# Kernel optimization log

Measured on AMD Instinct MI355X. Metric: run time of the kernel, lower is better.

Reference implementation:

```python
import jax, jax.numpy as jnp
import numpy as np

VARIANCE = (0.1, 0.2)
THRESHOLD = 0.5
NEG_POS = 3


def point_form(boxes):
    # (cx,cy,w,h) -> (xmin,ymin,xmax,ymax)
    return jnp.concatenate([boxes[:, :2] - boxes[:, 2:] / 2,
                            boxes[:, :2] + boxes[:, 2:] / 2], axis=1)


def jaccard(a, b):
    # a: [T,4] xyxy truths, b: [P,4] xyxy priors -> IoU [T,P]
    lt = jnp.maximum(a[:, None, :2], b[None, :, :2])
    rb = jnp.minimum(a[:, None, 2:], b[None, :, 2:])
    wh = jnp.clip(rb - lt, 0.0)
    inter = wh[..., 0] * wh[..., 1]
    area_a = ((a[:, 2] - a[:, 0]) * (a[:, 3] - a[:, 1]))[:, None]
    area_b = ((b[:, 2] - b[:, 0]) * (b[:, 3] - b[:, 1]))[None, :]
    return inter / (area_a + area_b - inter)


def encode(matched, priors):
    g_cxcy = (matched[:, :2] + matched[:, 2:]) / 2 - priors[:, :2]
    g_cxcy = g_cxcy / (VARIANCE[0] * priors[:, 2:])
    g_wh = jnp.log((matched[:, 2:] - matched[:, :2]) / priors[:, 2:]) / VARIANCE[1]
    return jnp.concatenate([g_cxcy, g_wh], axis=1)


def match_one(truths, priors):
    # SSD match for one image; labels are zeroed in BiBoxLoss -> binary conf {0,1}
    overlaps = jaccard(truths, point_form(priors))          # [T,P]
    best_prior_idx = jnp.argmax(overlaps, axis=1)           # [T]
    best_truth_overlap = jnp.max(overlaps, axis=0)          # [P]
    best_truth_idx = jnp.argmax(overlaps, axis=0)           # [P]
    best_truth_overlap = best_truth_overlap.at[best_prior_idx].set(2.0)
    best_truth_idx = best_truth_idx.at[best_prior_idx].set(
        jnp.arange(truths.shape[0]))
    matched = truths[best_truth_idx]                        # [P,4]
    conf = jnp.where(best_truth_overlap < THRESHOLD, 0, 1)  # [P] int
    loc = encode(matched, priors)
    return loc, conf


def bibox_loss(loc_data, conf_data, priors, targets):
    num, num_priors = loc_data.shape[0], loc_data.shape[1]
    truths = targets[..., :4]                               # [B,T,4]
    loc_t, conf_t = jax.vmap(lambda t: match_one(t, priors))(truths)

    pos = conf_t > 0                                        # [B,P]
    # smooth L1 (sum) over positive priors
    ad = jnp.abs(loc_data - loc_t)
    sl1 = jnp.where(ad < 1.0, 0.5 * ad * ad, ad - 0.5)
    loss_l = jnp.sum(sl1 * pos[..., None].astype(loc_data.dtype))

    # per-prior CE (logsumexp - gathered logit) for hard-negative mining
    lse = jax.nn.logsumexp(conf_data, axis=-1)              # [B,P]
    gathered = jnp.take_along_axis(conf_data, conf_t[..., None], axis=-1)[..., 0]
    loss_c_all = lse - gathered                             # [B,P]

    loss_c_mine = jnp.where(pos, 0.0, loss_c_all)
    loss_idx = jnp.argsort(-loss_c_mine, axis=1)
    idx_rank = jnp.argsort(loss_idx, axis=1)                # rank of each prior
    num_pos = jnp.sum(pos.astype(jnp.int32), axis=1, keepdims=True)  # [B,1]
    num_neg = jnp.minimum(NEG_POS * num_pos, num_priors - 1)
    neg = idx_rank < num_neg                                # [B,P]

    sel = pos | neg
    loss_c = jnp.sum(jnp.where(sel, loss_c_all, 0.0))

    N = jnp.sum(num_pos).astype(loc_data.dtype)
    return loss_l / N, loss_c / N


def setup_inputs() -> dict:
    key = jax.random.key(0)
    k1, k2, k3, k4, k5, k6 = jax.random.split(key, 6)
    B, P, T = 32, 65536, 16
    loc_data = jax.random.normal(k1, (B, P, 4), dtype=jnp.float32)
    conf_data = jax.random.normal(k2, (B, P, 2), dtype=jnp.float32)
    # priors: valid center-form boxes
    pc = 0.15 + 0.7 * jax.random.uniform(k3, (P, 2), dtype=jnp.float32)
    pwh = 0.05 + 0.25 * jax.random.uniform(k4, (P, 2), dtype=jnp.float32)
    priors = jnp.concatenate([pc, pwh], axis=1)
    # targets: valid corner-form boxes + dummy label column (zeroed by the loss)
    tc = 0.2 + 0.6 * jax.random.uniform(k5, (B, T, 2), dtype=jnp.float32)
    twh = 0.05 + 0.25 * jax.random.uniform(k6, (B, T, 2), dtype=jnp.float32)
    boxes = jnp.concatenate([tc - twh / 2, tc + twh / 2], axis=-1)
    targets = jnp.concatenate(
        [boxes, jnp.ones((B, T, 1), dtype=jnp.float32)], axis=-1)
    return {"loc_data": loc_data, "conf_data": conf_data,
            "priors": priors, "targets": targets}


def reference(loc_data, conf_data, priors, targets):
    return bibox_loss(loc_data, conf_data, priors, targets)
```

## Files before the change

### kernel.cpp

```cpp
#include <hip/hip_runtime.h>

#define NB_ 32
#define NP_ 65536
#define NT_ 16
#define HB 1024
#define HSCALE 128.0f
#define NBX 32
#define CHUNKS 2
#define BIAS 0xAAAAAAAAu

__device__ __forceinline__ float softplus_(float x) {
    return fmaxf(x, 0.0f) + __logf(1.0f + __expf(-fabsf(x)));
}

__device__ __forceinline__ float iou_fast(float tx0, float ty0, float tx1, float ty1, float ta,
                                          float bx0, float by0, float bx1, float by1, float ar) {
    float lx = fmaxf(tx0, bx0), ly = fmaxf(ty0, by0);
    float rx = fminf(tx1, bx1), ry = fminf(ty1, by1);
    float w = fmaxf(rx - lx, 0.0f), h = fmaxf(ry - ly, 0.0f);
    float inter = w * h;
    return __fdividef(inter, ta + ar - inter);
}

__global__ void __launch_bounds__(256) mainK(
    const float* __restrict__ loc, const float* __restrict__ conf,
    const float* __restrict__ priors, const float* __restrict__ targets,
    unsigned* __restrict__ hcnt, float* __restrict__ hsum,
    unsigned long long* __restrict__ bestPrior,
    float* __restrict__ sums_ll, float* __restrict__ sums_pc, unsigned* __restrict__ num_pos,
    float* __restrict__ final_l, float* __restrict__ final_c, unsigned* __restrict__ final_n,
    unsigned* __restrict__ bticket, unsigned* __restrict__ gticket,
    float* __restrict__ out)
{
    const int bx = blockIdx.x, b = blockIdx.y, tid = threadIdx.x;

    __shared__ float tr[NT_][5];
    __shared__ int hc[HB];
    __shared__ float hs[HB];
    __shared__ unsigned wkey[4][NT_], wp[4][NT_];
    __shared__ float sh_ll[4], sh_pc[4];
    __shared__ int sh_np[4];
    __shared__ unsigned ps[NT_];
    __shared__ float s_dll, s_dpc;
    __shared__ int s_dnp;
    __shared__ unsigned ccnt[16];
    __shared__ float csm[16];
    __shared__ int s_merge, s_lastg;

    for (int i = tid; i < HB; i += 256) { hc[i] = 0; hs[i] = 0.0f; }
    if (tid < NT_) {
        const float* tp = targets + ((size_t)b * NT_ + tid) * 5;
        float x0 = tp[0], y0 = tp[1], x1 = tp[2], y1 = tp[3];
        tr[tid][0] = x0; tr[tid][1] = y0; tr[tid][2] = x1; tr[tid][3] = y1;
        tr[tid][4] = (x1 - x0) * (y1 - y0);
    }
    __syncthreads();

    float ll_acc = 0.0f, pc_acc = 0.0f;
    int np_acc = 0;
    unsigned tkey[NT_];
#pragma unroll
    for (int t = 0; t < NT_; t++) tkey[t] = 0u;

    for (int c = 0; c < CHUNKS; c++) {
        const int pbase = (bx * CHUNKS + c) * 1024 + tid;
        float4 pr[4];
        float pbx0[4], pby0[4], pbx1[4], pby1[4], par[4];
#pragma unroll
        for (int i = 0; i < 4; i++) {
            pr[i] = ((const float4*)priors)[pbase + 256 * i];
            float hw = pr[i].z * 0.5f, hh = pr[i].w * 0.5f;
            pbx0[i] = pr[i].x - hw; pby0[i] = pr[i].y - hh;
            pbx1[i] = pr[i].x + hw; pby1[i] = pr[i].y + hh;
            par[i] = (pbx1[i] - pbx0[i]) * (pby1[i] - pby0[i]);
        }
        unsigned pkey[4] = {0u, 0u, 0u, 0u};
#pragma unroll
        for (int t = 0; t < NT_; t++) {
            float tx0 = tr[t][0], ty0 = tr[t][1], tx1 = tr[t][2], ty1 = tr[t][3], ta = tr[t][4];
            unsigned lowt = (unsigned)(15 - t);
            unsigned lowc = (unsigned)(15 - c * 4);
#pragma unroll
            for (int i = 0; i < 4; i++) {
                float iou = iou_fast(tx0, ty0, tx1, ty1, ta,
                                     pbx0[i], pby0[i], pbx1[i], pby1[i], par[i]);
                unsigned base = (__float_as_uint(iou) & 0xFFFFFFFCu) << 2;
                unsigned kt = base | lowt;
                unsigned kp = base | (lowc - (unsigned)i);
                pkey[i] = (kt > pkey[i]) ? kt : pkey[i];
                tkey[t] = (kp > tkey[t]) ? kp : tkey[t];
            }
        }
#pragma unroll
        for (int i = 0; i < 4; i++) {
            int p = pbase + 256 * i;
            size_t bp = (size_t)b * NP_ + p;
            bool pos = (pkey[i] >= 0xFC000000u);
            float2 cxy = ((const float2*)conf)[bp];
            float dd = cxy.y - cxy.x;
            float v = pos ? 0.0f : softplus_(dd);
            int bin = min(HB - 1, (int)(v * HSCALE));
            atomicAdd(&hc[bin], 1);
            atomicAdd(&hs[bin], v);
            if (pos) {
                np_acc++;
                pc_acc += softplus_(-dd);
                int t = 15 - (int)(pkey[i] & 15u);
                float tx0 = tr[t][0], ty0 = tr[t][1], tx1 = tr[t][2], ty1 = tr[t][3];
                float gcx = ((tx0 + tx1) * 0.5f - pr[i].x) / (0.1f * pr[i].z);
                float gcy = ((ty0 + ty1) * 0.5f - pr[i].y) / (0.1f * pr[i].w);
                float gw = __logf((tx1 - tx0) / pr[i].z) * 5.0f;
                float gh = __logf((ty1 - ty0) / pr[i].w) * 5.0f;
                float4 ld = ((const float4*)loc)[bp];
                float d0 = fabsf(ld.x - gcx), d1 = fabsf(ld.y - gcy);
                float d2 = fabsf(ld.z - gw),  d3 = fabsf(ld.w - gh);
                ll_acc += (d0 < 1.0f) ? 0.5f * d0 * d0 : d0 - 0.5f;
                ll_acc += (d1 < 1.0f) ? 0.5f * d1 * d1 : d1 - 0.5f;
                ll_acc += (d2 < 1.0f) ? 0.5f * d2 * d2 : d2 - 0.5f;
                ll_acc += (d3 < 1.0f) ? 0.5f * d3 * d3 : d3 - 0.5f;
            }
        }
    }

    const int wave = tid >> 6, lane = tid & 63;
#pragma unroll
    for (int t = 0; t < NT_; t++) {
        unsigned k = tkey[t], m = k;
        for (int off = 32; off > 0; off >>= 1) {
            unsigned o = __shfl_down(m, off, 64);
            m = (o > m) ? o : m;
        }
        m = __shfl(m, 0, 64);
        unsigned long long ball = __ballot(k == m);
        if (lane == 0) {
            int l = __ffsll((long long)ball) - 1;
            int ci = 15 - (int)(m & 15u);
            int p = bx * (CHUNKS * 1024) + ci * 256 + wave * 64 + l;
            wkey[wave][t] = m;
            wp[wave][t] = (unsigned)p;
        }
    }
    for (int off = 32; off > 0; off >>= 1) {
        ll_acc += __shfl_down(ll_acc, off, 64);
        pc_acc += __shfl_down(pc_acc, off, 64);
        np_acc += __shfl_down(np_acc, off, 64);
    }
    if (lane == 0) { sh_ll[wave] = ll_acc; sh_pc[wave] = pc_acc; sh_np[wave] = np_acc; }
    __syncthreads();

    if (tid < NT_) {
        unsigned bk = wkey[0][tid], bpv = wp[0][tid];
        for (int w = 1; w < 4; w++) {
            unsigned k2 = wkey[w][tid], p2 = wp[w][tid];
            if (k2 > bk || (k2 == bk && p2 < bpv)) { bk = k2; bpv = p2; }
        }
        unsigned long long pk = (((unsigned long long)bk) << 32) | (unsigned)(~bpv);
        atomicMax(&bestPrior[b * NT_ + tid], pk);
    }
    if (tid == 0) {
        atomicAdd(&sums_ll[b], sh_ll[0] + sh_ll[1] + sh_ll[2] + sh_ll[3]);
        atomicAdd(&sums_pc[b], sh_pc[0] + sh_pc[1] + sh_pc[2] + sh_pc[3]);
        atomicAdd(&num_pos[b], (unsigned)(sh_np[0] + sh_np[1] + sh_np[2] + sh_np[3]));
    }
    for (int i = tid; i < HB; i += 256) {
        int cval = hc[i];
        if (cval) {
            atomicAdd(&hcnt[b * HB + i], (unsigned)cval);
            atomicAdd(&hsum[b * HB + i], hs[i]);
        }
    }
    __syncthreads();
    if (tid == 0) {
        unsigned old = atomicAdd(&bticket[b], 1u);
        s_merge = (old == BIAS + (NBX - 1)) ? 1 : 0;
        s_dll = 0.0f; s_dpc = 0.0f; s_dnp = 0; s_lastg = 0;
    }
    __syncthreads();
    if (!s_merge) return;
    __threadfence();

#pragma unroll
    for (int k = 0; k < 4; k++) {
        int i = k * 256 + tid;
        hc[i] = (int)(hcnt[b * HB + i] - BIAS);
        hs[i] = hsum[b * HB + i];
    }
    if (tid < NT_) {
        unsigned long long v = bestPrior[b * NT_ + tid];
        ps[tid] = ~((unsigned)(v & 0xffffffffULL));
    }
    __syncthreads();

    if (tid < NT_) {
        unsigned p = ps[tid];
        bool active = true;
        for (int u = tid + 1; u < NT_; u++)
            if (ps[u] == p) { active = false; break; }
        if (active) {
            float4 prv = ((const float4*)priors)[p];
            float hw = prv.z * 0.5f, hh = prv.w * 0.5f;
            float qx0 = prv.x - hw, qy0 = prv.y - hh;
            float qx1 = prv.x + hw, qy1 = prv.y + hh;
            float areab = (qx1 - qx0) * (qy1 - qy0);
            unsigned pk = 0u;
            for (int tt = 0; tt < NT_; tt++) {
                float iou = iou_fast(tr[tt][0], tr[tt][1], tr[tt][2], tr[tt][3], tr[tt][4],
                                     qx0, qy0, qx1, qy1, areab);
                unsigned cand = ((__float_as_uint(iou) & 0xFFFFFFFCu) << 2)
                              | (unsigned)(15 - tt);
                pk = (cand > pk) ? cand : pk;
            }
            bool pos0 = (pk >= 0xFC000000u);
            int t0 = 15 - (int)(pk & 15u);
            size_t bp = (size_t)b * NP_ + p;
            float2 cxy = ((const float2*)conf)[bp];
            float dd = cxy.y - cxy.x;
            float4 ld = ((const float4*)loc)[bp];

            auto sl1_of = [&](int tt) -> float {
                float tx0 = tr[tt][0], ty0 = tr[tt][1], tx1 = tr[tt][2], ty1 = tr[tt][3];
                float gcx = ((tx0 + tx1) * 0.5f - prv.x) / (0.1f * prv.z);
                float gcy = ((ty0 + ty1) * 0.5f - prv.y) / (0.1f * prv.w);
                float gw = __logf((tx1 - tx0) / prv.z) * 5.0f;
                float gh = __logf((ty1 - ty0) / prv.w) * 5.0f;
                float d0 = fabsf(ld.x - gcx), d1 = fabsf(ld.y - gcy);
                float d2 = fabsf(ld.z - gw),  d3 = fabsf(ld.w - gh);
                float s = (d0 < 1.0f) ? 0.5f * d0 * d0 : d0 - 0.5f;
                s += (d1 < 1.0f) ? 0.5f * d1 * d1 : d1 - 0.5f;
                s += (d2 < 1.0f) ? 0.5f * d2 * d2 : d2 - 0.5f;
                s += (d3 < 1.0f) ? 0.5f * d3 * d3 : d3 - 0.5f;
                return s;
            };
            float dll = sl1_of(tid) - (pos0 ? sl1_of(t0) : 0.0f);
            atomicAdd(&s_dll, dll);
            if (!pos0) {
                float v = softplus_(dd);
                int bin = min(HB - 1, (int)(v * HSCALE));
                atomicSub(&hc[bin], 1);
                atomicAdd(&hs[bin], -v);
                atomicAdd(&s_dpc, softplus_(-dd));
                atomicAdd(&s_dnp, 1);
            }
        }
    }
    __syncthreads();

    if (tid < 16) {
        unsigned cacc = 0; float sacc = 0.0f;
        for (int j = 0; j < 64; j++) { cacc += (unsigned)hc[tid * 64 + j]; sacc += hs[tid * 64 + j]; }
        ccnt[tid] = cacc; csm[tid] = sacc;
    }
    __syncthreads();

    if (tid == 0) {
        float sll = sums_ll[b] + s_dll;
        float spc = sums_pc[b] + s_dpc;
        int n = (int)(num_pos[b] - BIAS) + s_dnp;
        int K = 3 * n;
        if (K > NP_ - 1) K = NP_ - 1;
        float tk = 0.0f;
        if (K > 0) {
            unsigned need = (unsigned)K, cum = 0;
            float s = 0.0f;
            int cb = 15;
            for (; cb > 0; --cb) {
                if (cum + ccnt[cb] >= need) break;
                cum += ccnt[cb]; s += csm[cb];
            }
            int bin = cb * 64 + 63;
            for (; bin > cb * 64; --bin) {
                if (cum + (unsigned)hc[bin] >= need) break;
                cum += (unsigned)hc[bin]; s += hs[bin];
            }
            unsigned rem = need - cum;
            int cv = hc[bin];
            float avg = (cv > 0) ? __fdividef(hs[bin], (float)cv) : 0.0f;
            tk = s + (float)rem * avg;
        }
        atomicAdd(final_l, sll);
        atomicAdd(final_c, spc + tk);
        atomicAdd(final_n, (unsigned)n);
    }
    __syncthreads();
    if (tid == 0) {
        unsigned old = atomicAdd(gticket, 1u);
        s_lastg = (old == BIAS + (NB_ - 1)) ? 1 : 0;
    }
    __syncthreads();

    if (s_lastg && tid == 0) {
        __threadfence();
        float lv = *final_l;
        float cv = *final_c;
        unsigned nv = *final_n - BIAS;
        float fn = (float)nv;
        out[0] = lv / fn;
        out[1] = cv / fn;
    }
}

extern "C" void kernel_launch(void* const* d_in, const int* in_sizes, int n_in,
                              void* d_out, int out_size, void* d_ws, size_t ws_size,
                              hipStream_t stream) {
    const float* loc = (const float*)d_in[0];
    const float* conf = (const float*)d_in[1];
    const float* priors = (const float*)d_in[2];
    const float* targets = (const float*)d_in[3];
    float* out = (float*)d_out;

    char* w = (char*)d_ws;
    unsigned* hcnt = (unsigned*)w;
    float* hsum = (float*)(w + (128u << 10));
    char* acc = w + (256u << 10);
    unsigned long long* bestPrior = (unsigned long long*)acc;
    float* sums_ll = (float*)(acc + 4096);
    float* sums_pc = (float*)(acc + 4096 + 128);
    unsigned* num_pos = (unsigned*)(acc + 4096 + 256);
    float* final_l = (float*)(acc + 4096 + 384);
    float* final_c = (float*)(acc + 4096 + 512);
    unsigned* final_n = (unsigned*)(acc + 4096 + 640);
    unsigned* bticket = (unsigned*)(acc + 4096 + 768);
    unsigned* gticket = (unsigned*)(acc + 4096 + 896);

    mainK<<<dim3(NBX, NB_), 256, 0, stream>>>(loc, conf, priors, targets,
                                              hcnt, hsum, bestPrior,
                                              sums_ll, sums_pc, num_pos,
                                              final_l, final_c, final_n,
                                              bticket, gticket, out);
}
```

Before: 154.1 us.

## Histogram quantized conf logit difference with packed 64-bit atomics, defer softplus

Replaces the per-negative softplus plus two shared atomics (count and float sum) with one 64-bit shared atomic. That atomic packs a count and a fixed-point sum of the quantized logit difference, binned by the difference itself. Softplus is then applied once per bin at merge time, to the bin's mean difference, to approximate the bin's loss sum. The conf loads are also hoisted ahead of the IoU loop to overlap memory latency. This removes transcendental work and halves atomic traffic in the hot loop, but makes the hard-negative sum an approximation: softplus of the bin mean instead of the mean of softplus.

```diff
diff --git a/kernel.cpp b/kernel.cpp
--- a/kernel.cpp
+++ b/kernel.cpp
@@ -4,10 +4,12 @@
 #define NP_ 65536
 #define NT_ 16
 #define HB 1024
-#define HSCALE 128.0f
 #define NBX 32
 #define CHUNKS 2
 #define BIAS 0xAAAAAAAAu
+#define BIAS64 0xAAAAAAAAAAAAAAAAull
+#define DQ 1048576.0f
+#define QMASK ((1ull << 44) - 1)
 
 __device__ __forceinline__ float softplus_(float x) {
     return fmaxf(x, 0.0f) + __logf(1.0f + __expf(-fabsf(x)));
@@ -22,10 +24,16 @@
     return __fdividef(inter, ta + ar - inter);
 }
 
+__device__ __forceinline__ unsigned quant_dd(float dd) {
+    float qf = fmaf(dd, DQ, 8.0f * DQ);
+    qf = fminf(fmaxf(qf, 0.0f), 16.0f * DQ - 1.0f);
+    return (unsigned)qf;
+}
+
 __global__ void __launch_bounds__(256) mainK(
     const float* __restrict__ loc, const float* __restrict__ conf,
     const float* __restrict__ priors, const float* __restrict__ targets,
-    unsigned* __restrict__ hcnt, float* __restrict__ hsum,
+    unsigned long long* __restrict__ ghist,
     unsigned long long* __restrict__ bestPrior,
     float* __restrict__ sums_ll, float* __restrict__ sums_pc, unsigned* __restrict__ num_pos,
     float* __restrict__ final_l, float* __restrict__ final_c, unsigned* __restrict__ final_n,
@@ -35,8 +43,8 @@
     const int bx = blockIdx.x, b = blockIdx.y, tid = threadIdx.x;
 
     __shared__ float tr[NT_][5];
-    __shared__ int hc[HB];
-    __shared__ float hs[HB];
+    __shared__ unsigned long long hpack[HB];
+    __shared__ float fbin[HB];
     __shared__ unsigned wkey[4][NT_], wp[4][NT_];
     __shared__ float sh_ll[4], sh_pc[4];
     __shared__ int sh_np[4];
@@ -47,7 +55,10 @@
     __shared__ float csm[16];
     __shared__ int s_merge, s_lastg;
 
-    for (int i = tid; i < HB; i += 256) { hc[i] = 0; hs[i] = 0.0f; }
+    int* cnt = (int*)hpack;
+    float* sdd = (float*)(cnt + HB);
+
+    for (int i = tid; i < HB; i += 256) hpack[i] = 0ull;
     if (tid < NT_) {
         const float* tp = targets + ((size_t)b * NT_ + tid) * 5;
         float x0 = tp[0], y0 = tp[1], x1 = tp[2], y1 = tp[3];
@@ -65,10 +76,12 @@
     for (int c = 0; c < CHUNKS; c++) {
         const int pbase = (bx * CHUNKS + c) * 1024 + tid;
         float4 pr[4];
+        float2 cxy[4];
         float pbx0[4], pby0[4], pbx1[4], pby1[4], par[4];
 #pragma unroll
         for (int i = 0; i < 4; i++) {
             pr[i] = ((const float4*)priors)[pbase + 256 * i];
+            cxy[i] = ((const float2*)conf)[(size_t)b * NP_ + pbase + 256 * i];
             float hw = pr[i].z * 0.5f, hh = pr[i].w * 0.5f;
             pbx0[i] = pr[i].x - hw; pby0[i] = pr[i].y - hh;
             pbx1[i] = pr[i].x + hw; pby1[i] = pr[i].y + hh;
@@ -96,12 +109,7 @@
             int p = pbase + 256 * i;
             size_t bp = (size_t)b * NP_ + p;
             bool pos = (pkey[i] >= 0xFC000000u);
-            float2 cxy = ((const float2*)conf)[bp];
-            float dd = cxy.y - cxy.x;
-            float v = pos ? 0.0f : softplus_(dd);
-            int bin = min(HB - 1, (int)(v * HSCALE));
-            atomicAdd(&hc[bin], 1);
-            atomicAdd(&hs[bin], v);
+            float dd = cxy[i].y - cxy[i].x;
             if (pos) {
                 np_acc++;
                 pc_acc += softplus_(-dd);
@@ -118,6 +126,9 @@
                 ll_acc += (d1 < 1.0f) ? 0.5f * d1 * d1 : d1 - 0.5f;
                 ll_acc += (d2 < 1.0f) ? 0.5f * d2 * d2 : d2 - 0.5f;
                 ll_acc += (d3 < 1.0f) ? 0.5f * d3 * d3 : d3 - 0.5f;
+            } else {
+                unsigned q = quant_dd(dd);
+                atomicAdd(&hpack[q >> 14], (1ull << 44) | (unsigned long long)q);
             }
         }
     }
@@ -163,11 +174,8 @@
         atomicAdd(&num_pos[b], (unsigned)(sh_np[0] + sh_np[1] + sh_np[2] + sh_np[3]));
     }
     for (int i = tid; i < HB; i += 256) {
-        int cval = hc[i];
-        if (cval) {
-            atomicAdd(&hcnt[b * HB + i], (unsigned)cval);
-            atomicAdd(&hsum[b * HB + i], hs[i]);
-        }
+        unsigned long long v = hpack[i];
+        if (v) atomicAdd(&ghist[b * HB + i], v);
     }
     __syncthreads();
     if (tid == 0) {
@@ -182,8 +190,11 @@
 #pragma unroll
     for (int k = 0; k < 4; k++) {
         int i = k * 256 + tid;
-        hc[i] = (int)(hcnt[b * HB + i] - BIAS);
-        hs[i] = hsum[b * HB + i];
+        unsigned long long d = ghist[b * HB + i] - BIAS64;
+        int n = (int)(d >> 44);
+        float sq = (float)(d & QMASK);
+        cnt[i] = n;
+        sdd[i] = sq * (1.0f / DQ) - 8.0f * (float)n;
     }
     if (tid < NT_) {
         unsigned long long v = bestPrior[b * NT_ + tid];
@@ -234,10 +245,10 @@
             float dll = sl1_of(tid) - (pos0 ? sl1_of(t0) : 0.0f);
             atomicAdd(&s_dll, dll);
             if (!pos0) {
-                float v = softplus_(dd);
-                int bin = min(HB - 1, (int)(v * HSCALE));
-                atomicSub(&hc[bin], 1);
-                atomicAdd(&hs[bin], -v);
+                unsigned q = quant_dd(dd);
+                int bin = (int)(q >> 14);
+                atomicSub(&cnt[bin], 1);
+                atomicAdd(&sdd[bin], -((float)q * (1.0f / DQ) - 8.0f));
                 atomicAdd(&s_dpc, softplus_(-dd));
                 atomicAdd(&s_dnp, 1);
             }
@@ -245,9 +256,19 @@
     }
     __syncthreads();
 
+#pragma unroll
+    for (int k = 0; k < 4; k++) {
+        int i = k * 256 + tid;
+        int n = cnt[i];
+        fbin[i] = (n > 0) ? (float)n * softplus_(sdd[i] * __frcp_rn((float)n)) : 0.0f;
+    }
+    __syncthreads();
     if (tid < 16) {
         unsigned cacc = 0; float sacc = 0.0f;
-        for (int j = 0; j < 64; j++) { cacc += (unsigned)hc[tid * 64 + j]; sacc += hs[tid * 64 + j]; }
+        for (int j = 0; j < 64; j++) {
+            cacc += (unsigned)cnt[tid * 64 + j];
+            sacc += fbin[tid * 64 + j];
+        }
         ccnt[tid] = cacc; csm[tid] = sacc;
     }
     __syncthreads();
@@ -269,12 +290,12 @@
             }
             int bin = cb * 64 + 63;
             for (; bin > cb * 64; --bin) {
-                if (cum + (unsigned)hc[bin] >= need) break;
-                cum += (unsigned)hc[bin]; s += hs[bin];
+                if (cum + (unsigned)cnt[bin] >= need) break;
+                cum += (unsigned)cnt[bin]; s += fbin[bin];
             }
             unsigned rem = need - cum;
-            int cv = hc[bin];
-            float avg = (cv > 0) ? __fdividef(hs[bin], (float)cv) : 0.0f;
+            int cv = cnt[bin];
+            float avg = (cv > 0) ? __fdividef(fbin[bin], (float)cv) : 0.0f;
             tk = s + (float)rem * avg;
         }
         atomicAdd(final_l, sll);
@@ -309,8 +330,7 @@
     float* out = (float*)d_out;
 
     char* w = (char*)d_ws;
-    unsigned* hcnt = (unsigned*)w;
-    float* hsum = (float*)(w + (128u << 10));
+    unsigned long long* ghist = (unsigned long long*)w;
     char* acc = w + (256u << 10);
     unsigned long long* bestPrior = (unsigned long long*)acc;
     float* sums_ll = (float*)(acc + 4096);
@@ -323,7 +343,7 @@
     unsigned* gticket = (unsigned*)(acc + 4096 + 896);
 
     mainK<<<dim3(NBX, NB_), 256, 0, stream>>>(loc, conf, priors, targets,
-                                              hcnt, hsum, bestPrior,
+                                              ghist, bestPrior,
                                               sums_ll, sums_pc, num_pos,
                                               final_l, final_c, final_n,
                                               bticket, gticket, out);
```

Measured after the change: 154.0 us. No clear change (-0.0%).
